# Optimization experiments

Measured on AMD Instinct MI355X. Metric: run time of the kernel, lower is better.

Reference implementation:

```python
import jax, jax.numpy as jnp
import numpy as np

# ---- 4-wire quantum gate: RX(x_w + theta_w) per wire, CNOT ring, <Z_w> per wire ----
N_WIRES = 4
DIM = 2 ** N_WIRES  # 16 statevector amplitudes

def _cnot_perm_inv():
    # CNOTs (0,1),(1,2),(2,3),(3,0) applied sequentially permute computational basis states.
    # inv[j] = k such that basis state k maps to j; then psi_new = psi_old[inv].
    inv = np.zeros(DIM, dtype=np.int32)
    for k in range(DIM):
        b = [(k >> 3) & 1, (k >> 2) & 1, (k >> 1) & 1, k & 1]  # wire 0 = MSB
        b[1] ^= b[0]; b[2] ^= b[1]; b[3] ^= b[2]; b[0] ^= b[3]
        nk = (b[0] << 3) | (b[1] << 2) | (b[2] << 1) | b[3]
        inv[nk] = k
    return jnp.asarray(inv)

_PERM = _cnot_perm_inv()
# sign[k, w] = (-1)^{bit_w(k)} for PauliZ expectation on wire w
_ZSIGN = jnp.asarray(np.array([[1.0 - 2.0 * ((k >> (3 - w)) & 1) for w in range(N_WIRES)]
                               for k in range(DIM)], dtype=np.float32))  # [16, 4]

def _qgate(angles, theta):
    # angles: [B, 4]. Encoder RX(x_w) then trainable RX(theta_w) on the same wire = RX(x_w + theta_w).
    a = (angles + theta) * 0.5
    c, s = jnp.cos(a), jnp.sin(a)
    amp = jnp.stack([c + 0j, (-1j) * s], axis=-1)  # [B, 4, 2] per-wire RX|0> amplitudes
    # product state over 4 wires -> [B, 16]
    psi = jnp.einsum('bi,bj,bk,bl->bijkl', amp[:, 0], amp[:, 1], amp[:, 2], amp[:, 3]).reshape(-1, DIM)
    psi = psi[:, _PERM]  # CNOT ring (classical basis permutation)
    probs = jnp.real(psi * jnp.conj(psi))  # [B, 16]
    return probs @ _ZSIGN  # [B, 4] PauliZ expectations


def setup_inputs() -> dict:
    key = jax.random.key(0)
    T, B, D, H, Q = 256, 2048, 128, 4, 4
    ks = jax.random.split(key, 16)
    inp = {"inputs": jax.random.normal(ks[0], (T, B, D), dtype=jnp.float32)}
    bound = 1.0 / float(np.sqrt(D + H))  # torch Linear default init range
    for j, n in enumerate(["f", "i", "u", "o"]):
        inp["W" + n] = jax.random.uniform(ks[1 + j], (Q, D + H), jnp.float32, -bound, bound)
        inp["b" + n] = jax.random.uniform(ks[5 + j], (Q,), jnp.float32, -bound, bound)
        inp["th" + n] = jax.random.normal(ks[9 + j], (Q,), dtype=jnp.float32)  # trainable RX angles
    return inp


def reference(inputs, Wf, bf, Wi, bi, Wu, bu, Wo, bo, thf, thi, thu, tho):
    B = inputs.shape[1]
    H = N_WIRES  # hidden_dim == n_qubits == 4
    h0 = jnp.zeros((B, H), dtype=inputs.dtype)
    c0 = jnp.zeros((B, H), dtype=inputs.dtype)

    def step(carry, x):
        hx, cx = carry
        comb = jnp.concatenate([x, hx], axis=1)  # [B, D+H]
        f = jax.nn.sigmoid(_qgate(comb @ Wf.T + bf, thf))
        i = jax.nn.sigmoid(_qgate(comb @ Wi.T + bi, thi))
        g = jnp.tanh(_qgate(comb @ Wu.T + bu, thu))
        o = jax.nn.sigmoid(_qgate(comb @ Wo.T + bo, tho))
        cx = f * cx + i * g
        hx = o * jnp.tanh(cx)
        return (hx, cx), hx

    (hx, cx), stacked = jax.lax.scan(step, (h0, c0), inputs)
    return (stacked, hx, cx)
```

## Files before the change

### kernel.cpp

```cpp
#include <hip/hip_runtime.h>

#define TT 256
#define BB 2048
#define DIN 128
#define DWROW 132
#define INV2PI 0.15915494309189535f
#define LOG2E  1.4426950408889634f

__device__ __forceinline__ const float* rfl_ptr(const float* p) {
    unsigned long long u = (unsigned long long)p;
    unsigned lo = __builtin_amdgcn_readfirstlane((unsigned)u);
    unsigned hi = __builtin_amdgcn_readfirstlane((unsigned)(u >> 32));
    return (const float*)(((unsigned long long)hi << 32) | lo);
}

#define DPP_BCAST(dst, src, j) \
    dst = __int_as_float(__builtin_amdgcn_update_dpp( \
        0, __float_as_int(src), (j) * 0x55, 0xF, 0xF, true))

__device__ __forceinline__ float sigm(float x) {
    float e = __builtin_amdgcn_exp2f(-LOG2E * x);
    return __builtin_amdgcn_rcpf(1.0f + e);
}
__device__ __forceinline__ float tanh_f(float x) {
    float e = __builtin_amdgcn_exp2f((2.0f * LOG2E) * x);
    return 1.0f - 2.0f * __builtin_amdgcn_rcpf(1.0f + e);
}

__global__ __launch_bounds__(256) void qlstm_phase1(
    const float* __restrict__ x,
    const float* __restrict__ Wf, const float* __restrict__ bf, const float* __restrict__ thf,
    const float* __restrict__ Wi, const float* __restrict__ bi, const float* __restrict__ thi,
    const float* __restrict__ Wu, const float* __restrict__ bu, const float* __restrict__ thu,
    const float* __restrict__ Wo, const float* __restrict__ bo, const float* __restrict__ tho,
    float* __restrict__ Ax)
{
    __shared__ float xT[DIN][65];

    const int tid = threadIdx.x;
    const size_t tile = blockIdx.x;

    const float4* xg = (const float4*)x + tile * (64 * DIN / 4);
#pragma unroll
    for (int i = 0; i < 8; ++i) {
        int f   = i * 256 + tid;
        int row = f >> 5;
        int c4  = f & 31;
        float4 v = xg[f];
        xT[4 * c4 + 0][row] = v.x;
        xT[4 * c4 + 1][row] = v.y;
        xT[4 * c4 + 2][row] = v.z;
        xT[4 * c4 + 3][row] = v.w;
    }
    __syncthreads();

    const int wv   = tid >> 6;
    const int lane = tid & 63;

    const float* Wp  = (wv == 0) ? Wf  : (wv == 1) ? Wi  : (wv == 2) ? Wu  : Wo;
    const float* bp  = (wv == 0) ? bf  : (wv == 1) ? bi  : (wv == 2) ? bu  : bo;
    const float* thp = (wv == 0) ? thf : (wv == 1) ? thi : (wv == 2) ? thu : tho;
    const float* Wg  = rfl_ptr(Wp);
    const float* bg  = rfl_ptr(bp);
    const float* thg = rfl_ptr(thp);

    float acc0 = bg[0] + thg[0];
    float acc1 = bg[1] + thg[1];
    float acc2 = bg[2] + thg[2];
    float acc3 = bg[3] + thg[3];

#pragma unroll 8
    for (int j = 0; j < DIN; ++j) {
        float xv = xT[j][lane];
        acc0 = fmaf(xv, Wg[0 * DWROW + j], acc0);
        acc1 = fmaf(xv, Wg[1 * DWROW + j], acc1);
        acc2 = fmaf(xv, Wg[2 * DWROW + j], acc2);
        acc3 = fmaf(xv, Wg[3 * DWROW + j], acc3);
    }

    float4 o;
    o.x = acc0 * INV2PI; o.y = acc1 * INV2PI;
    o.z = acc2 * INV2PI; o.w = acc3 * INV2PI;
    ((float4*)Ax)[(tile * 64 + lane) * 4 + wv] = o;
}

__global__ __launch_bounds__(64) void qlstm_phase2(
    const float* __restrict__ Ax,
    const float* __restrict__ Wf, const float* __restrict__ Wi,
    const float* __restrict__ Wu, const float* __restrict__ Wo,
    float* __restrict__ out)
{
    const int gtid = blockIdx.x * 64 + threadIdx.x;
    const int w = gtid & 3;
    const int b = gtid >> 2;

    const float* Ws[4] = {Wf, Wi, Wu, Wo};
    float wh[4][4];
#pragma unroll
    for (int g = 0; g < 4; ++g)
#pragma unroll
        for (int j = 0; j < 4; ++j)
            wh[g][j] = Ws[g][w * DWROW + DIN + j] * INV2PI;

    const size_t S = (size_t)BB * 16;
    const float* ap = Ax + (size_t)b * 16 + w;

    float ar[4][4];
#pragma unroll
    for (int d = 0; d < 4; ++d)
#pragma unroll
        for (int g = 0; g < 4; ++g)
            ar[d][g] = ap[(size_t)d * S + g * 4];

    float hv0 = 0.f, hv1 = 0.f, hv2 = 0.f, hv3 = 0.f;
    float cst = 0.f;
    float h   = 0.f;

    for (int t4 = 0; t4 < TT / 4; ++t4) {
#pragma unroll
        for (int k = 0; k < 4; ++k) {
            const int t = 4 * t4 + k;
            float a0 = ar[k][0], a1 = ar[k][1], a2 = ar[k][2], a3 = ar[k][3];
            int tn = t + 4; if (tn > TT - 1) tn = TT - 1;
#pragma unroll
            for (int g = 0; g < 4; ++g)
                ar[k][g] = ap[(size_t)tn * S + g * 4];

            float z[4];
#pragma unroll
            for (int g = 0; g < 4; ++g) {
                float ang = (g == 0) ? a0 : (g == 1) ? a1 : (g == 2) ? a2 : a3;
                ang = fmaf(hv0, wh[g][0], ang);
                ang = fmaf(hv1, wh[g][1], ang);
                ang = fmaf(hv2, wh[g][2], ang);
                ang = fmaf(hv3, wh[g][3], ang);
                z[g] = __builtin_amdgcn_cosf(ang);
            }

            float G[4];
#pragma unroll
            for (int g = 0; g < 4; ++g) {
                float q0, q1, q2, q3;
                DPP_BCAST(q0, z[g], 0);
                DPP_BCAST(q1, z[g], 1);
                DPP_BCAST(q2, z[g], 2);
                DPP_BCAST(q3, z[g], 3);
                float p01   = q0 * q1;
                float p012  = p01 * q2;
                float p0123 = p012 * q3;
                float c0    = q1 * q2 * q3;
                G[g] = (w == 0) ? c0 : (w == 1) ? p01 : (w == 2) ? p012 : p0123;
            }

            float fg = sigm(G[0]);
            float ig = sigm(G[1]);
            float ug = tanh_f(G[2]);
            float og = sigm(G[3]);

            cst = fmaf(fg, cst, ig * ug);
            float th = tanh_f(cst);
            h = og * th;

            out[(size_t)t * (BB * 4) + b * 4 + w] = h;

            DPP_BCAST(hv0, h, 0);
            DPP_BCAST(hv1, h, 1);
            DPP_BCAST(hv2, h, 2);
            DPP_BCAST(hv3, h, 3);
        }
    }

    out[(size_t)TT * BB * 4 + b * 4 + w]          = h;
    out[(size_t)TT * BB * 4 + BB * 4 + b * 4 + w] = cst;
}

extern "C" void kernel_launch(void* const* d_in, const int* in_sizes, int n_in,
                              void* d_out, int out_size, void* d_ws, size_t ws_size,
                              hipStream_t stream)
{
    const float* x   = (const float*)d_in[0];
    const float* Wf  = (const float*)d_in[1];
    const float* bf  = (const float*)d_in[2];
    const float* thf = (const float*)d_in[3];
    const float* Wi  = (const float*)d_in[4];
    const float* bi  = (const float*)d_in[5];
    const float* thi = (const float*)d_in[6];
    const float* Wu  = (const float*)d_in[7];
    const float* bu  = (const float*)d_in[8];
    const float* thu = (const float*)d_in[9];
    const float* Wo  = (const float*)d_in[10];
    const float* bo  = (const float*)d_in[11];
    const float* tho = (const float*)d_in[12];
    float* Ax   = (float*)d_ws;
    float* outp = (float*)d_out;

    qlstm_phase1<<<dim3((TT * BB) / 64), dim3(256), 0, stream>>>(
        x, Wf, bf, thf, Wi, bi, thi, Wu, bu, thu, Wo, bo, tho, Ax);
    qlstm_phase2<<<dim3((BB * 4) / 64), dim3(64), 0, stream>>>(
        Ax, Wf, Wi, Wu, Wo, outp);
}
```

Measured before the change: 468.8 us.

## Split recurrent phase across gate×wire lanes with swizzle exchange of activations

The recurrent kernel now assigns one lane per (batch, gate, wire) instead of per (batch, wire). Each lane computes a single gate angle, cosine, product and activation, using a unified sigmoid/tanh form. Activations are exchanged across the gate groups with ds_swizzle, and the cell update runs redundantly, with only one group writing output. This quadruples the parallelism and shortens the per-step serial chain, at the cost of swizzle latency and redundant work.

```diff
diff --git a/kernel.cpp b/kernel.cpp
--- a/kernel.cpp
+++ b/kernel.cpp
@@ -18,10 +18,9 @@
     dst = __int_as_float(__builtin_amdgcn_update_dpp( \
         0, __float_as_int(src), (j) * 0x55, 0xF, 0xF, true))
 
-__device__ __forceinline__ float sigm(float x) {
-    float e = __builtin_amdgcn_exp2f(-LOG2E * x);
-    return __builtin_amdgcn_rcpf(1.0f + e);
-}
+#define SWZ(dst, src, imm) \
+    dst = __int_as_float(__builtin_amdgcn_ds_swizzle(__float_as_int(src), (imm)))
+
 __device__ __forceinline__ float tanh_f(float x) {
     float e = __builtin_amdgcn_exp2f((2.0f * LOG2E) * x);
     return 1.0f - 2.0f * __builtin_amdgcn_rcpf(1.0f + e);
@@ -92,25 +91,26 @@
 {
     const int gtid = blockIdx.x * 64 + threadIdx.x;
     const int w = gtid & 3;
-    const int b = gtid >> 2;
+    const int g = (gtid >> 2) & 3;
+    const int b = gtid >> 4;
 
-    const float* Ws[4] = {Wf, Wi, Wu, Wo};
-    float wh[4][4];
-#pragma unroll
-    for (int g = 0; g < 4; ++g)
-#pragma unroll
-        for (int j = 0; j < 4; ++j)
-            wh[g][j] = Ws[g][w * DWROW + DIN + j] * INV2PI;
+    const float* Wrow = (g == 0) ? Wf : (g == 1) ? Wi : (g == 2) ? Wu : Wo;
+    const float wh0 = Wrow[w * DWROW + DIN + 0] * INV2PI;
+    const float wh1 = Wrow[w * DWROW + DIN + 1] * INV2PI;
+    const float wh2 = Wrow[w * DWROW + DIN + 2] * INV2PI;
+    const float wh3 = Wrow[w * DWROW + DIN + 3] * INV2PI;
+
+    const float kk = (g == 2) ? (2.0f * LOG2E) : (-LOG2E);
+    const float Aa = (g == 2) ? 1.0f : 0.0f;
+    const float Bb = (g == 2) ? -2.0f : 1.0f;
 
     const size_t S = (size_t)BB * 16;
-    const float* ap = Ax + (size_t)b * 16 + w;
+    const float* ap = Ax + (size_t)b * 16 + (g * 4 + w);
 
-    float ar[4][4];
+    float ar[4];
 #pragma unroll
     for (int d = 0; d < 4; ++d)
-#pragma unroll
-        for (int g = 0; g < 4; ++g)
-            ar[d][g] = ap[(size_t)d * S + g * 4];
+        ar[d] = ap[(size_t)d * S];
 
     float hv0 = 0.f, hv1 = 0.f, hv2 = 0.f, hv3 = 0.f;
     float cst = 0.f;
@@ -120,48 +120,41 @@
 #pragma unroll
         for (int k = 0; k < 4; ++k) {
             const int t = 4 * t4 + k;
-            float a0 = ar[k][0], a1 = ar[k][1], a2 = ar[k][2], a3 = ar[k][3];
+            float a = ar[k];
             int tn = t + 4; if (tn > TT - 1) tn = TT - 1;
-#pragma unroll
-            for (int g = 0; g < 4; ++g)
-                ar[k][g] = ap[(size_t)tn * S + g * 4];
+            ar[k] = ap[(size_t)tn * S];
 
-            float z[4];
-#pragma unroll
-            for (int g = 0; g < 4; ++g) {
-                float ang = (g == 0) ? a0 : (g == 1) ? a1 : (g == 2) ? a2 : a3;
-                ang = fmaf(hv0, wh[g][0], ang);
-                ang = fmaf(hv1, wh[g][1], ang);
-                ang = fmaf(hv2, wh[g][2], ang);
-                ang = fmaf(hv3, wh[g][3], ang);
-                z[g] = __builtin_amdgcn_cosf(ang);
-            }
+            float m23 = fmaf(hv2, wh2, hv3 * wh3);
+            float ang = fmaf(hv0, wh0, fmaf(hv1, wh1, a)) + m23;
+            float z   = __builtin_amdgcn_cosf(ang);
 
-            float G[4];
-#pragma unroll
-            for (int g = 0; g < 4; ++g) {
-                float q0, q1, q2, q3;
-                DPP_BCAST(q0, z[g], 0);
-                DPP_BCAST(q1, z[g], 1);
-                DPP_BCAST(q2, z[g], 2);
-                DPP_BCAST(q3, z[g], 3);
-                float p01   = q0 * q1;
-                float p012  = p01 * q2;
-                float p0123 = p012 * q3;
-                float c0    = q1 * q2 * q3;
-                G[g] = (w == 0) ? c0 : (w == 1) ? p01 : (w == 2) ? p012 : p0123;
-            }
+            float q0, q1, q2, q3;
+            DPP_BCAST(q0, z, 0);
+            DPP_BCAST(q1, z, 1);
+            DPP_BCAST(q2, z, 2);
+            DPP_BCAST(q3, z, 3);
+            float t23 = q2 * q3;
+            float p01 = q0 * q1;
+            float G = (w == 0) ? q1 * t23
+                    : (w == 1) ? p01
+                    : (w == 2) ? p01 * q2
+                    :            p01 * t23;
 
-            float fg = sigm(G[0]);
-            float ig = sigm(G[1]);
-            float ug = tanh_f(G[2]);
-            float og = sigm(G[3]);
+            float e   = __builtin_amdgcn_exp2f(kk * G);
+            float act = fmaf(Bb, __builtin_amdgcn_rcpf(1.0f + e), Aa);
 
-            cst = fmaf(fg, cst, ig * ug);
+            float fa, ia, ua, oa;
+            SWZ(fa, act, 0x013);
+            SWZ(ia, act, 0x093);
+            SWZ(ua, act, 0x113);
+            SWZ(oa, act, 0x193);
+
+            cst = fmaf(fa, cst, ia * ua);
             float th = tanh_f(cst);
-            h = og * th;
+            h = oa * th;
 
-            out[(size_t)t * (BB * 4) + b * 4 + w] = h;
+            if (g == 0)
+                out[(size_t)t * (BB * 4) + b * 4 + w] = h;
 
             DPP_BCAST(hv0, h, 0);
             DPP_BCAST(hv1, h, 1);
@@ -170,8 +163,10 @@
         }
     }
 
-    out[(size_t)TT * BB * 4 + b * 4 + w]          = h;
-    out[(size_t)TT * BB * 4 + BB * 4 + b * 4 + w] = cst;
+    if (g == 0) {
+        out[(size_t)TT * BB * 4 + b * 4 + w]          = h;
+        out[(size_t)TT * BB * 4 + BB * 4 + b * 4 + w] = cst;
+    }
 }
 
 extern "C" void kernel_launch(void* const* d_in, const int* in_sizes, int n_in,
@@ -196,6 +191,6 @@
 
     qlstm_phase1<<<dim3((TT * BB) / 64), dim3(256), 0, stream>>>(
         x, Wf, bf, thf, Wi, bi, thi, Wu, bu, thu, Wo, bo, tho, Ax);
-    qlstm_phase2<<<dim3((BB * 4) / 64), dim3(64), 0, stream>>>(
+    qlstm_phase2<<<dim3((BB * 16) / 64), dim3(64), 0, stream>>>(
         Ax, Wf, Wi, Wu, Wo, outp);
 }
```

New measurement: 440.9 us. 1.06x faster.
